# Performance work log

Hardware: AMD Instinct MI355X
Metric: run time of the kernel (lower is better)

Reference implementation:

```python
import jax, jax.numpy as jnp
import numpy as np


def setup_inputs() -> dict:
    key = jax.random.key(0)
    ks = jax.random.split(key, 7)
    B, P, D = 4, 2048, 1024
    s = 1.0 / np.sqrt(D)
    return {
        "x":  jax.random.normal(ks[0], (B, P, D), dtype=jnp.float32),
        "Wq": jax.random.normal(ks[1], (D, D), dtype=jnp.float32) * s,
        "bq": jnp.zeros((D,), dtype=jnp.float32),
        "Wk": jax.random.normal(ks[2], (D, D), dtype=jnp.float32) * s,
        "bk": jnp.zeros((D,), dtype=jnp.float32),
        "Wv": jax.random.normal(ks[3], (D, D), dtype=jnp.float32) * s,
        "bv": jnp.zeros((D,), dtype=jnp.float32),
    }


def reference(x, Wq, bq, Wk, bk, Wv, bv):
    # x: [B, P, D]; Linear uses W stored torch-style [out, in]: y = x @ W.T + b
    b, p, d = x.shape
    q = jnp.einsum("bpd,ed->bpe", x, Wq) + bq
    k = jnp.einsum("bpd,ed->bpe", x, Wk) + bk
    v = jnp.einsum("bpd,ed->bpe", x, Wv) + bv
    attn = jnp.einsum("bqd,bkd->bqk", q, k)  # [B, P, P]
    causal = jnp.triu(jnp.ones((p, p), dtype=bool), k=1)  # True above diagonal
    attn = jnp.where(causal, -jnp.inf, attn)
    attn = attn / jnp.sqrt(jnp.asarray(d, dtype=attn.dtype))
    scores = jax.nn.softmax(attn, axis=-1)
    # dropout is identity in eval/deterministic mode
    return jnp.einsum("bqk,bkd->bqd", scores, v)
```

## Files before the change

kernel.cpp:

```cpp
#include <hip/hip_runtime.h>
#include <hip/hip_bf16.h>


typedef __attribute__((ext_vector_type(8))) short bf16x8;
typedef __attribute__((ext_vector_type(4))) float f32x4;

__device__ __forceinline__ unsigned short f2bf(float f) {
    union { float f; unsigned u; } v; v.f = f;
    unsigned r = v.u + 0x7FFF + ((v.u >> 16) & 1);
    return (unsigned short)(r >> 16);
}

__device__ __forceinline__ void gload_lds16(const unsigned short* g, unsigned short* l) {
    __builtin_amdgcn_global_load_lds(
        (const __attribute__((address_space(1))) unsigned int*)g,
        (__attribute__((address_space(3))) unsigned int*)l, 16, 0, 0);
}

__global__ void convert_kernel(const float* __restrict__ x,  const float* __restrict__ wq,
                               const float* __restrict__ wk, const float* __restrict__ wv,
                               const float* __restrict__ bq, const float* __restrict__ bk,
                               const float* __restrict__ bv,
                               unsigned short* __restrict__ xb, unsigned short* __restrict__ wqkvb,
                               float* __restrict__ bqkv, float* __restrict__ lsum) {
    long t = (long)blockIdx.x * blockDim.x + threadIdx.x;
    long idx = t * 4;
    const float* src; unsigned short* dst; long off;
    if      (idx <  8388608) { src = x;  dst = xb;            off = idx;            }
    else if (idx <  9437184) { src = wq; dst = wqkvb;         off = idx -  8388608; }
    else if (idx < 10485760) { src = wk; dst = wqkvb+1048576; off = idx -  9437184; }
    else if (idx < 11534336) { src = wv; dst = wqkvb+2097152; off = idx - 10485760; }
    else return;
    float4 v = *(const float4*)(src + off);
    ushort4 o = make_ushort4(f2bf(v.x), f2bf(v.y), f2bf(v.z), f2bf(v.w));
    *(ushort4*)(dst + off) = o;
    if (t < 768) {
        long o2 = t * 4;
        float4 b;
        if      (o2 < 1024) b = *(const float4*)(bq + o2);
        else if (o2 < 2048) b = *(const float4*)(bk + o2 - 1024);
        else                b = *(const float4*)(bv + o2 - 2048);
        *(float4*)(bqkv + o2) = b;
    }
    if (t >= 1024 && t < 3072) {
        float4 z = make_float4(0.f, 0.f, 0.f, 0.f);
        *(float4*)(lsum + (t - 1024) * 4) = z;
    }
}

__global__ void transpose_v(const unsigned short* __restrict__ V,
                            unsigned short* __restrict__ VT) {
    __shared__ unsigned short t[64][72];
    const int p0 = blockIdx.x * 64;
    const int e0 = blockIdx.y * 64;
    const int r = threadIdx.x >> 3;
    const int c = (threadIdx.x & 7) * 8;
    const unsigned short* src = V + (long)(p0 + r) * 3072 + e0 + c;
    *(int4*)&t[r][c]      = *(const int4*)src;
    *(int4*)&t[r + 32][c] = *(const int4*)(src + 32 * 3072);
    __syncthreads();
    unsigned short ov[8];
    unsigned short* dst = VT + (long)(e0 + r) * 8192 + p0 + c;
#pragma unroll
    for (int j = 0; j < 8; ++j) ov[j] = t[c + j][r];
    *(int4*)dst = *(int4*)ov;
    dst = VT + (long)(e0 + r + 32) * 8192 + p0 + c;
#pragma unroll
    for (int j = 0; j < 8; ++j) ov[j] = t[c + j][r + 32];
    *(int4*)dst = *(int4*)ov;
}

template<int MODE>
__global__ __launch_bounds__(128, 2)
void gemm_bt(const unsigned short* __restrict__ A, int lda,
             const unsigned short* __restrict__ B, int ldb,
             unsigned short* __restrict__ Cb, float* __restrict__ Cf, int ldc,
             const float* __restrict__ bias_col, float* __restrict__ lsum,
             int K, long bsA, long bsB, long bsC, long bsL) {
    const int n0 = blockIdx.x * 128;
    const int m0 = blockIdx.y * 128;
    if (MODE == 1 && n0 > m0) return;
    const int z = blockIdx.z;
    A += (long)z * bsA;
    B += (long)z * bsB;
    if (MODE == 2) Cf += (long)z * bsC; else Cb += (long)z * bsC;
    if (MODE != 0) lsum += (long)z * bsL;

    const int Keff = (MODE == 2) ? (m0 + 128) : K;

    __shared__ unsigned short As[128 * 64];
    __shared__ unsigned short Bs[128 * 64];

    const int tid  = threadIdx.x;
    const int lane = tid & 63;
    const int w    = tid >> 6;
    const int q    = lane >> 4;
    const int ln   = lane & 15;

    const int srow = lane >> 3;
    const int sc   = (lane & 7) ^ (srow & 7);
    const unsigned short* gA = A + (long)(m0 + w * 64 + srow) * lda + sc * 8;
    const unsigned short* gB = B + (long)(n0 + w * 64 + srow) * ldb + sc * 8;
    unsigned short* lA = &As[(w * 64) * 64];
    unsigned short* lB = &Bs[(w * 64) * 64];

    const int pr0 = ((q)     ^ (ln & 7)) * 8;
    const int pr1 = ((q + 4) ^ (ln & 7)) * 8;

    f32x4 acc[4][8] = {};

    for (int k0 = 0; k0 < Keff; k0 += 64) {
        __syncthreads();
#pragma unroll
        for (int s = 0; s < 8; ++s) {
            gload_lds16(gA + k0 + (long)(s * 8) * lda, lA + (s * 8) * 64);
            gload_lds16(gB + k0 + (long)(s * 8) * ldb, lB + (s * 8) * 64);
        }
        __syncthreads();
#pragma unroll
        for (int kk = 0; kk < 2; ++kk) {
            const int pr = kk ? pr1 : pr0;
            bf16x8 af[4], bfr[8];
#pragma unroll
            for (int i = 0; i < 4; ++i)
                af[i] = *(const bf16x8*)(&As[(w * 64 + i * 16 + ln) * 64 + pr]);
#pragma unroll
            for (int j = 0; j < 8; ++j)
                bfr[j] = *(const bf16x8*)(&Bs[(j * 16 + ln) * 64 + pr]);
#pragma unroll
            for (int i = 0; i < 4; ++i)
#pragma unroll
                for (int j = 0; j < 8; ++j)
                    acc[i][j] = __builtin_amdgcn_mfma_f32_16x16x32_bf16(bfr[j], af[i], acc[i][j], 0, 0, 0);
        }
    }

    if (MODE == 0) {
#pragma unroll
        for (int j = 0; j < 8; ++j) {
            const float4 bc = *(const float4*)(bias_col + n0 + j * 16 + q * 4);
#pragma unroll
            for (int i = 0; i < 4; ++i) {
                const int m = m0 + w * 64 + i * 16 + ln;
                const int n = n0 + j * 16 + q * 4;
                ushort4 o = make_ushort4(f2bf(acc[i][j][0] + bc.x), f2bf(acc[i][j][1] + bc.y),
                                         f2bf(acc[i][j][2] + bc.z), f2bf(acc[i][j][3] + bc.w));
                *(ushort4*)(Cb + (long)m * ldc + n) = o;
            }
        }
    } else if (MODE == 1) {
        const float scale = 0.03125f;
        float rs[4] = {0.f, 0.f, 0.f, 0.f};
#pragma unroll
        for (int i = 0; i < 4; ++i) {
            const int m = m0 + w * 64 + i * 16 + ln;
#pragma unroll
            for (int j = 0; j < 8; ++j) {
                const int n = n0 + j * 16 + q * 4;
                float p0 = (n     <= m) ? __expf(acc[i][j][0] * scale) : 0.f;
                float p1 = (n + 1 <= m) ? __expf(acc[i][j][1] * scale) : 0.f;
                float p2 = (n + 2 <= m) ? __expf(acc[i][j][2] * scale) : 0.f;
                float p3 = (n + 3 <= m) ? __expf(acc[i][j][3] * scale) : 0.f;
                rs[i] += (p0 + p1) + (p2 + p3);
                ushort4 o = make_ushort4(f2bf(p0), f2bf(p1), f2bf(p2), f2bf(p3));
                *(ushort4*)(Cb + (long)m * ldc + n) = o;
            }
        }
#pragma unroll
        for (int i = 0; i < 4; ++i) {
            float s = rs[i];
            s += __shfl_xor(s, 16); s += __shfl_xor(s, 32);
            if (lane < 16) atomicAdd(&lsum[m0 + w * 64 + i * 16 + ln], s);
        }
    } else {
#pragma unroll
        for (int i = 0; i < 4; ++i) {
            const int m = m0 + w * 64 + i * 16 + ln;
            const float inv = 1.0f / lsum[m];
#pragma unroll
            for (int j = 0; j < 8; ++j) {
                const int n = n0 + j * 16 + q * 4;
                float4 o = make_float4(acc[i][j][0] * inv, acc[i][j][1] * inv,
                                       acc[i][j][2] * inv, acc[i][j][3] * inv);
                *(float4*)(Cf + (long)m * ldc + n) = o;
            }
        }
    }
}

extern "C" void kernel_launch(void* const* d_in, const int* in_sizes, int n_in,
                              void* d_out, int out_size, void* d_ws, size_t ws_size,
                              hipStream_t stream) {
    const float* x  = (const float*)d_in[0];
    const float* Wq = (const float*)d_in[1];
    const float* bq = (const float*)d_in[2];
    const float* Wk = (const float*)d_in[3];
    const float* bk = (const float*)d_in[4];
    const float* Wv = (const float*)d_in[5];
    const float* bv = (const float*)d_in[6];
    float* out = (float*)d_out;

    char* ws = (char*)d_ws;
    unsigned short* xb    = (unsigned short*)ws;
    unsigned short* VTb   = (unsigned short*)ws;
    ws += (long)8192 * 1024 * 2;
    unsigned short* wqkvb = (unsigned short*)ws; ws += (long)3072 * 1024 * 2;
    float*          bqkv  = (float*)ws;          ws += (long)3072 * 4;
    float*          lsum  = (float*)ws;          ws += (long)8192 * 4;
    unsigned short* QKVb  = (unsigned short*)ws; ws += (long)8192 * 3072 * 2;
    unsigned short* Pb    = (unsigned short*)ws; ws += (long)4 * 2048 * 2048 * 2;

    hipLaunchKernelGGL(convert_kernel, dim3(11264), dim3(256), 0, stream,
                       x, Wq, Wk, Wv, bq, bk, bv, xb, wqkvb, bqkv, lsum);

    hipLaunchKernelGGL((gemm_bt<0>), dim3(24, 64, 1), dim3(128), 0, stream,
                       xb, 1024, wqkvb, 1024, QKVb, (float*)nullptr, 3072,
                       bqkv, (float*)nullptr, 1024, 0L, 0L, 0L, 0L);

    hipLaunchKernelGGL(transpose_v, dim3(128, 16, 1), dim3(256), 0, stream,
                       QKVb + 2048, VTb);

    hipLaunchKernelGGL((gemm_bt<1>), dim3(16, 16, 4), dim3(128), 0, stream,
                       QKVb, 3072, QKVb + 1024, 3072, Pb, (float*)nullptr, 2048,
                       (const float*)nullptr, lsum,
                       1024, (long)2048 * 3072, (long)2048 * 3072, (long)2048 * 2048, 2048L);

    hipLaunchKernelGGL((gemm_bt<2>), dim3(8, 16, 4), dim3(128), 0, stream,
                       Pb, 2048, VTb, 8192, (unsigned short*)nullptr, out, 1024,
                       (const float*)nullptr, lsum,
                       2048, (long)2048 * 2048, 2048L, (long)2048 * 1024, 2048L);
}
```

Before: 266.4 us.

## Fuse V transpose into QKV GEMM, use 4-wave tiles and triangular grid

The QKV projection GEMM now writes V directly in transposed layout, so the separate transpose kernel and its extra round trip through memory are gone. All GEMMs move from 2 waves to 4 waves per 128x128 tile, each wave owning a 64x64 subtile, which lowers per-wave accumulator registers and changes occupancy. The QK^T launch uses a compact triangular grid of 136 tiles per batch instead of launching the full square and returning early. The transposed V stores are scalar 2-byte writes strided by 8192 elements, which may coalesce poorly in the projection epilogue.

After: 264.6 us. Within noise of the previous version (-0.7%).

```diff
diff --git a/kernel.cpp b/kernel.cpp
--- a/kernel.cpp
+++ b/kernel.cpp
@@ -48,39 +48,25 @@
     }
 }
 
-__global__ void transpose_v(const unsigned short* __restrict__ V,
-                            unsigned short* __restrict__ VT) {
-    __shared__ unsigned short t[64][72];
-    const int p0 = blockIdx.x * 64;
-    const int e0 = blockIdx.y * 64;
-    const int r = threadIdx.x >> 3;
-    const int c = (threadIdx.x & 7) * 8;
-    const unsigned short* src = V + (long)(p0 + r) * 3072 + e0 + c;
-    *(int4*)&t[r][c]      = *(const int4*)src;
-    *(int4*)&t[r + 32][c] = *(const int4*)(src + 32 * 3072);
-    __syncthreads();
-    unsigned short ov[8];
-    unsigned short* dst = VT + (long)(e0 + r) * 8192 + p0 + c;
-#pragma unroll
-    for (int j = 0; j < 8; ++j) ov[j] = t[c + j][r];
-    *(int4*)dst = *(int4*)ov;
-    dst = VT + (long)(e0 + r + 32) * 8192 + p0 + c;
-#pragma unroll
-    for (int j = 0; j < 8; ++j) ov[j] = t[c + j][r + 32];
-    *(int4*)dst = *(int4*)ov;
-}
-
 template<int MODE>
-__global__ __launch_bounds__(128, 2)
+__global__ __launch_bounds__(256)
 void gemm_bt(const unsigned short* __restrict__ A, int lda,
              const unsigned short* __restrict__ B, int ldb,
              unsigned short* __restrict__ Cb, float* __restrict__ Cf, int ldc,
+             unsigned short* __restrict__ VTb,
              const float* __restrict__ bias_col, float* __restrict__ lsum,
              int K, long bsA, long bsB, long bsC, long bsL) {
-    const int n0 = blockIdx.x * 128;
-    const int m0 = blockIdx.y * 128;
-    if (MODE == 1 && n0 > m0) return;
-    const int z = blockIdx.z;
+    int m0, n0, z;
+    if (MODE == 1) {
+        const int t = blockIdx.x;
+        int i = (int)((sqrtf(8.0f * t + 1.0f) - 1.0f) * 0.5f);
+        while ((i + 1) * (i + 2) / 2 <= t) ++i;
+        while (i * (i + 1) / 2 > t) --i;
+        const int j = t - i * (i + 1) / 2;
+        m0 = i * 128; n0 = j * 128; z = blockIdx.y;
+    } else {
+        n0 = blockIdx.x * 128; m0 = blockIdx.y * 128; z = blockIdx.z;
+    }
     A += (long)z * bsA;
     B += (long)z * bsB;
     if (MODE == 2) Cf += (long)z * bsC; else Cb += (long)z * bsC;
@@ -94,58 +80,74 @@
     const int tid  = threadIdx.x;
     const int lane = tid & 63;
     const int w    = tid >> 6;
+    const int wr   = (w >> 1) * 64;
+    const int wc   = (w & 1) * 64;
     const int q    = lane >> 4;
     const int ln   = lane & 15;
 
     const int srow = lane >> 3;
-    const int sc   = (lane & 7) ^ (srow & 7);
-    const unsigned short* gA = A + (long)(m0 + w * 64 + srow) * lda + sc * 8;
-    const unsigned short* gB = B + (long)(n0 + w * 64 + srow) * ldb + sc * 8;
-    unsigned short* lA = &As[(w * 64) * 64];
-    unsigned short* lB = &Bs[(w * 64) * 64];
+    const int sc   = (lane & 7) ^ srow;
+    const unsigned short* gA = A + (long)(m0 + w * 32 + srow) * lda + sc * 8;
+    const unsigned short* gB = B + (long)(n0 + w * 32 + srow) * ldb + sc * 8;
 
     const int pr0 = ((q)     ^ (ln & 7)) * 8;
     const int pr1 = ((q + 4) ^ (ln & 7)) * 8;
 
-    f32x4 acc[4][8] = {};
+    f32x4 acc[4][4] = {};
 
     for (int k0 = 0; k0 < Keff; k0 += 64) {
         __syncthreads();
 #pragma unroll
-        for (int s = 0; s < 8; ++s) {
-            gload_lds16(gA + k0 + (long)(s * 8) * lda, lA + (s * 8) * 64);
-            gload_lds16(gB + k0 + (long)(s * 8) * ldb, lB + (s * 8) * 64);
+        for (int s = 0; s < 4; ++s) {
+            gload_lds16(gA + k0 + (long)(s * 8) * lda, &As[(w * 32 + s * 8) * 64]);
+            gload_lds16(gB + k0 + (long)(s * 8) * ldb, &Bs[(w * 32 + s * 8) * 64]);
         }
         __syncthreads();
 #pragma unroll
         for (int kk = 0; kk < 2; ++kk) {
             const int pr = kk ? pr1 : pr0;
-            bf16x8 af[4], bfr[8];
+            bf16x8 af[4], bfr[4];
 #pragma unroll
             for (int i = 0; i < 4; ++i)
-                af[i] = *(const bf16x8*)(&As[(w * 64 + i * 16 + ln) * 64 + pr]);
-#pragma unroll
-            for (int j = 0; j < 8; ++j)
-                bfr[j] = *(const bf16x8*)(&Bs[(j * 16 + ln) * 64 + pr]);
+                af[i] = *(const bf16x8*)(&As[(wr + i * 16 + ln) * 64 + pr]);
+#pragma unroll
+            for (int j = 0; j < 4; ++j)
+                bfr[j] = *(const bf16x8*)(&Bs[(wc + j * 16 + ln) * 64 + pr]);
 #pragma unroll
             for (int i = 0; i < 4; ++i)
 #pragma unroll
-                for (int j = 0; j < 8; ++j)
+                for (int j = 0; j < 4; ++j)
                     acc[i][j] = __builtin_amdgcn_mfma_f32_16x16x32_bf16(bfr[j], af[i], acc[i][j], 0, 0, 0);
         }
     }
 
     if (MODE == 0) {
-#pragma unroll
-        for (int j = 0; j < 8; ++j) {
-            const float4 bc = *(const float4*)(bias_col + n0 + j * 16 + q * 4);
-#pragma unroll
-            for (int i = 0; i < 4; ++i) {
-                const int m = m0 + w * 64 + i * 16 + ln;
-                const int n = n0 + j * 16 + q * 4;
-                ushort4 o = make_ushort4(f2bf(acc[i][j][0] + bc.x), f2bf(acc[i][j][1] + bc.y),
-                                         f2bf(acc[i][j][2] + bc.z), f2bf(acc[i][j][3] + bc.w));
-                *(ushort4*)(Cb + (long)m * ldc + n) = o;
+        if (n0 < 2048) {
+#pragma unroll
+            for (int j = 0; j < 4; ++j) {
+                const float4 bc = *(const float4*)(bias_col + n0 + wc + j * 16 + q * 4);
+#pragma unroll
+                for (int i = 0; i < 4; ++i) {
+                    const int m = m0 + wr + i * 16 + ln;
+                    const int n = n0 + wc + j * 16 + q * 4;
+                    ushort4 o = make_ushort4(f2bf(acc[i][j][0] + bc.x), f2bf(acc[i][j][1] + bc.y),
+                                             f2bf(acc[i][j][2] + bc.z), f2bf(acc[i][j][3] + bc.w));
+                    *(ushort4*)(Cb + (long)m * ldc + n) = o;
+                }
+            }
+        } else {
+#pragma unroll
+            for (int j = 0; j < 4; ++j) {
+                const float4 bc = *(const float4*)(bias_col + n0 + wc + j * 16 + q * 4);
+                const int e = n0 - 2048 + wc + j * 16 + q * 4;
+#pragma unroll
+                for (int i = 0; i < 4; ++i) {
+                    const int m = m0 + wr + i * 16 + ln;
+                    VTb[(long)(e    ) * 8192 + m] = f2bf(acc[i][j][0] + bc.x);
+                    VTb[(long)(e + 1) * 8192 + m] = f2bf(acc[i][j][1] + bc.y);
+                    VTb[(long)(e + 2) * 8192 + m] = f2bf(acc[i][j][2] + bc.z);
+                    VTb[(long)(e + 3) * 8192 + m] = f2bf(acc[i][j][3] + bc.w);
+                }
             }
         }
     } else if (MODE == 1) {
@@ -153,10 +155,10 @@
         float rs[4] = {0.f, 0.f, 0.f, 0.f};
 #pragma unroll
         for (int i = 0; i < 4; ++i) {
-            const int m = m0 + w * 64 + i * 16 + ln;
-#pragma unroll
-            for (int j = 0; j < 8; ++j) {
-                const int n = n0 + j * 16 + q * 4;
+            const int m = m0 + wr + i * 16 + ln;
+#pragma unroll
+            for (int j = 0; j < 4; ++j) {
+                const int n = n0 + wc + j * 16 + q * 4;
                 float p0 = (n     <= m) ? __expf(acc[i][j][0] * scale) : 0.f;
                 float p1 = (n + 1 <= m) ? __expf(acc[i][j][1] * scale) : 0.f;
                 float p2 = (n + 2 <= m) ? __expf(acc[i][j][2] * scale) : 0.f;
@@ -170,16 +172,16 @@
         for (int i = 0; i < 4; ++i) {
             float s = rs[i];
             s += __shfl_xor(s, 16); s += __shfl_xor(s, 32);
-            if (lane < 16) atomicAdd(&lsum[m0 + w * 64 + i * 16 + ln], s);
+            if (lane < 16) atomicAdd(&lsum[m0 + wr + i * 16 + ln], s);
         }
     } else {
 #pragma unroll
         for (int i = 0; i < 4; ++i) {
-            const int m = m0 + w * 64 + i * 16 + ln;
+            const int m = m0 + wr + i * 16 + ln;
             const float inv = 1.0f / lsum[m];
 #pragma unroll
-            for (int j = 0; j < 8; ++j) {
-                const int n = n0 + j * 16 + q * 4;
+            for (int j = 0; j < 4; ++j) {
+                const int n = n0 + wc + j * 16 + q * 4;
                 float4 o = make_float4(acc[i][j][0] * inv, acc[i][j][1] * inv,
                                        acc[i][j][2] * inv, acc[i][j][3] * inv);
                 *(float4*)(Cf + (long)m * ldc + n) = o;
@@ -201,32 +203,28 @@
     float* out = (float*)d_out;
 
     char* ws = (char*)d_ws;
-    unsigned short* xb    = (unsigned short*)ws;
-    unsigned short* VTb   = (unsigned short*)ws;
-    ws += (long)8192 * 1024 * 2;
+    unsigned short* xb    = (unsigned short*)ws; ws += (long)8192 * 1024 * 2;
     unsigned short* wqkvb = (unsigned short*)ws; ws += (long)3072 * 1024 * 2;
     float*          bqkv  = (float*)ws;          ws += (long)3072 * 4;
     float*          lsum  = (float*)ws;          ws += (long)8192 * 4;
-    unsigned short* QKVb  = (unsigned short*)ws; ws += (long)8192 * 3072 * 2;
+    unsigned short* QKb   = (unsigned short*)ws; ws += (long)8192 * 2048 * 2;
+    unsigned short* VTb   = (unsigned short*)ws; ws += (long)1024 * 8192 * 2;
     unsigned short* Pb    = (unsigned short*)ws; ws += (long)4 * 2048 * 2048 * 2;
 
     hipLaunchKernelGGL(convert_kernel, dim3(11264), dim3(256), 0, stream,
                        x, Wq, Wk, Wv, bq, bk, bv, xb, wqkvb, bqkv, lsum);
 
-    hipLaunchKernelGGL((gemm_bt<0>), dim3(24, 64, 1), dim3(128), 0, stream,
-                       xb, 1024, wqkvb, 1024, QKVb, (float*)nullptr, 3072,
+    hipLaunchKernelGGL((gemm_bt<0>), dim3(24, 64, 1), dim3(256), 0, stream,
+                       xb, 1024, wqkvb, 1024, QKb, (float*)nullptr, 2048, VTb,
                        bqkv, (float*)nullptr, 1024, 0L, 0L, 0L, 0L);
 
-    hipLaunchKernelGGL(transpose_v, dim3(128, 16, 1), dim3(256), 0, stream,
-                       QKVb + 2048, VTb);
-
-    hipLaunchKernelGGL((gemm_bt<1>), dim3(16, 16, 4), dim3(128), 0, stream,
-                       QKVb, 3072, QKVb + 1024, 3072, Pb, (float*)nullptr, 2048,
-                       (const float*)nullptr, lsum,
-                       1024, (long)2048 * 3072, (long)2048 * 3072, (long)2048 * 2048, 2048L);
-
-    hipLaunchKernelGGL((gemm_bt<2>), dim3(8, 16, 4), dim3(128), 0, stream,
+    hipLaunchKernelGGL((gemm_bt<1>), dim3(136, 4, 1), dim3(256), 0, stream,
+                       QKb, 2048, QKb + 1024, 2048, Pb, (float*)nullptr, 2048,
+                       (unsigned short*)nullptr, (const float*)nullptr, lsum,
+                       1024, (long)2048 * 2048, (long)2048 * 2048, (long)2048 * 2048, 2048L);
+
+    hipLaunchKernelGGL((gemm_bt<2>), dim3(8, 16, 4), dim3(256), 0, stream,
                        Pb, 2048, VTb, 8192, (unsigned short*)nullptr, out, 1024,
-                       (const float*)nullptr, lsum,
+                       (unsigned short*)nullptr, (const float*)nullptr, lsum,
                        2048, (long)2048 * 2048, 2048L, (long)2048 * 1024, 2048L);
 }
```
